# Performance work log

Measured on AMD Instinct MI355X. Metric: run time of the kernel, lower is better.

## Reference

```python
import jax, jax.numpy as jnp
import numpy as np
import math

IN_FEATURES = 256
OUT_FEATURES = 128
B, N = 4, 4096


def setup_inputs() -> dict:
    key = jax.random.key(0)
    ks = jax.random.split(key, 8)
    h = jax.random.normal(ks[0], (B, N, IN_FEATURES), dtype=jnp.float32)
    adj = jax.random.randint(ks[1], (B, N, N), 0, 2, dtype=jnp.int32)
    # Linear params (torch nn.Linear: y = x @ W.T + b)
    s = 1.0 / math.sqrt(IN_FEATURES)
    Wq = jax.random.uniform(ks[2], (OUT_FEATURES, IN_FEATURES), jnp.float32, -s, s)
    bq = jax.random.uniform(ks[3], (OUT_FEATURES,), jnp.float32, -s, s)
    Wk = jax.random.uniform(ks[4], (OUT_FEATURES, IN_FEATURES), jnp.float32, -s, s)
    bk = jax.random.uniform(ks[5], (OUT_FEATURES,), jnp.float32, -s, s)
    Wv = jax.random.uniform(ks[6], (OUT_FEATURES, IN_FEATURES), jnp.float32, -s, s)
    bv = jax.random.uniform(ks[7], (OUT_FEATURES,), jnp.float32, -s, s)
    return {"h": h, "adj": adj, "Wq": Wq, "bq": bq, "Wk": Wk, "bk": bk, "Wv": Wv, "bv": bv}


def reference(h, adj, Wq, bq, Wk, bk, Wv, bv):
    # QKV projections: [B, N, D]
    q = jnp.einsum('bnf,df->bnd', h, Wq) + bq
    k = jnp.einsum('bnf,df->bnd', h, Wk) + bk
    v = jnp.einsum('bnf,df->bnd', h, Wv) + bv
    # Dense scores [B, N, N], scaled
    scores = jnp.einsum('bnd,bmd->bnm', q, k) / math.sqrt(OUT_FEATURES)
    neg = jnp.float32(-9e15)
    scores = jnp.where(adj > 0, scores, neg)
    probs = jax.nn.softmax(scores, axis=-1)
    return jnp.einsum('bnm,bmd->bnd', probs, v)
```

## Files before the change

kernel.cpp:

```cpp
#include <hip/hip_runtime.h>
#include <stdint.h>
#include <math.h>

#define NB 4
#define NN 4096
#define NF 256
#define ND 128
#define KVB 32
#define NR (NB * NN)
#define QKVE ((size_t)NR * ND)

typedef __bf16 bf16x8 __attribute__((ext_vector_type(8)));
typedef __bf16 bf16x4v __attribute__((ext_vector_type(4)));
typedef float f32x4 __attribute__((ext_vector_type(4)));
typedef int i32x4 __attribute__((ext_vector_type(4)));
typedef unsigned short u16x4 __attribute__((ext_vector_type(4)));

__device__ __forceinline__ unsigned short f2bf(float f) {
    union { float f; uint32_t u; } v; v.f = f;
    uint32_t r = (v.u + 0x7FFFu + ((v.u >> 16) & 1u)) >> 16;
    return (unsigned short)r;
}
__device__ __forceinline__ bf16x8 lds_read16(const unsigned short* base, int byte_off) {
    return *reinterpret_cast<const bf16x8*>(reinterpret_cast<const char*>(base) + byte_off);
}
__device__ __forceinline__ void gld_lds16(const void* g, void* l) {
    __builtin_amdgcn_global_load_lds(
        (const __attribute__((address_space(1))) void*)g,
        (__attribute__((address_space(3))) void*)l, 16, 0, 0);
}

__global__ __launch_bounds__(256) void qkv_proj(
    const float* __restrict__ h,
    const float* __restrict__ Wq, const float* __restrict__ bq,
    const float* __restrict__ Wk, const float* __restrict__ bk,
    const float* __restrict__ Wv, const float* __restrict__ bv,
    unsigned short* __restrict__ qo, unsigned short* __restrict__ ko,
    unsigned short* __restrict__ vs, float qscale)
{
    __shared__ unsigned short h_lds[64 * 128];
    __shared__ unsigned short w_lds[128 * 128];

    const int tid = threadIdx.x;
    const int lane = tid & 63;
    const int proj = blockIdx.x >> 8;
    const int R0 = (blockIdx.x & 255) * 64;
    const int wv = tid >> 6;
    const int l15 = lane & 15;
    const int lhi = lane >> 4;

    const float* W    = proj == 0 ? Wq : (proj == 1 ? Wk : Wv);
    const float* bias = proj == 0 ? bq : (proj == 1 ? bk : bv);
    const float scale = proj == 0 ? qscale : 1.0f;

    f32x4 acc[8];
#pragma unroll
    for (int i = 0; i < 8; ++i) acc[i] = f32x4{0.f, 0.f, 0.f, 0.f};

    for (int kc = 0; kc < 2; ++kc) {
        const int c0 = kc * 128;
        __syncthreads();
#pragma unroll
        for (int p = 0; p < 8; ++p) {
            int i2 = p * 256 + tid;
            int row = i2 >> 5;
            int seg = i2 & 31;
            f32x4 hv = *reinterpret_cast<const f32x4*>(h + (size_t)(R0 + row) * NF + c0 + seg * 4);
            u16x4 hb;
            hb[0] = f2bf(hv[0]); hb[1] = f2bf(hv[1]); hb[2] = f2bf(hv[2]); hb[3] = f2bf(hv[3]);
            int byte = (row * 256 + seg * 8) ^ ((row & 7) << 4);
            *reinterpret_cast<u16x4*>(reinterpret_cast<char*>(h_lds) + byte) = hb;
        }
#pragma unroll
        for (int p = 0; p < 16; ++p) {
            int i2 = p * 256 + tid;
            int row = i2 >> 5;
            int seg = i2 & 31;
            f32x4 wv4 = *reinterpret_cast<const f32x4*>(W + (size_t)row * NF + c0 + seg * 4);
            u16x4 wb;
            wb[0] = f2bf(wv4[0]); wb[1] = f2bf(wv4[1]); wb[2] = f2bf(wv4[2]); wb[3] = f2bf(wv4[3]);
            int byte = (row * 256 + seg * 8) ^ ((row & 7) << 4);
            *reinterpret_cast<u16x4*>(reinterpret_cast<char*>(w_lds) + byte) = wb;
        }
        __syncthreads();
        const int arow = 16 * wv + l15;
#pragma unroll
        for (int ks = 0; ks < 4; ++ks) {
            int k = ks * 32 + 8 * lhi;
            bf16x8 a = lds_read16(h_lds, (arow * 256 + k * 2) ^ ((arow & 7) << 4));
#pragma unroll
            for (int cs = 0; cs < 8; ++cs) {
                int d = 16 * cs + l15;
                bf16x8 b = lds_read16(w_lds, (d * 256 + k * 2) ^ ((d & 7) << 4));
                acc[cs] = __builtin_amdgcn_mfma_f32_16x16x32_bf16(a, b, acc[cs], 0, 0, 0);
            }
        }
    }
    if (proj < 2) {
        unsigned short* out = proj == 0 ? qo : ko;
#pragma unroll
        for (int cs = 0; cs < 8; ++cs) {
            int d = 16 * cs + l15;
            float bb = bias[d];
#pragma unroll
            for (int j = 0; j < 4; ++j) {
                int row = R0 + 16 * wv + 4 * lhi + j;
                out[(size_t)row * ND + d] = f2bf((acc[cs][j] + bb) * scale);
            }
        }
    } else {
        const int bb_ = R0 >> 12;
        const int nb_ = (R0 & (NN - 1)) + 16 * wv + 4 * lhi;
        const int pt = nb_ >> 5;
        const int ch = (nb_ >> 3) & 3;
        const int mm0 = nb_ & 7;
#pragma unroll
        for (int cs = 0; cs < 8; ++cs) {
            int d = 16 * cs + l15;
            float bb = bias[d];
            u16x4 o;
#pragma unroll
            for (int j = 0; j < 4; ++j) o[j] = f2bf(acc[cs][j] + bb);
            size_t oidx = ((size_t)(bb_ * 128 + pt)) * 4096 + ch * 1024 + d * 8 + mm0;
            *reinterpret_cast<u16x4*>(vs + oidx) = o;
        }
    }
}

__global__ __launch_bounds__(256, 2) void attn(
    const unsigned short* __restrict__ Q,
    const unsigned short* __restrict__ K,
    const unsigned short* __restrict__ VS,
    const int* __restrict__ adj,
    float* __restrict__ out,
    float* __restrict__ opart1,
    float* __restrict__ ml,
    int ntl)
{
    __shared__ unsigned short stA[8192];
    __shared__ unsigned short stB[8192];
    __shared__ unsigned short p_lds[4096];

    const int tid = threadIdx.x;
    const int lane = tid & 63;
    const int w = tid >> 6;
    const int l15 = lane & 15;
    const int lhi = lane >> 4;

    const int flat = blockIdx.x;
    const int x = flat & 7;
    const int rest = flat >> 3;
    const int qt = rest & 31;
    const int s2 = rest >> 5;
    const int combo = x + 8 * s2;
    const int b = combo & 3;
    const int sp = combo >> 2;
    const int q0w = qt * 128 + w * 32;
    const size_t bN = (size_t)b * NN;
    const int ptbase = sp * ntl;

    const unsigned short* Kb = K + bN * ND;
    const unsigned short* Vbase = VS + (size_t)b * 128 * 4096;
    const int* adjb = adj + (size_t)b * NN * NN + (size_t)(q0w + l15) * NN + 4 * lhi;

    bf16x8 qf[2][4];
#pragma unroll
    for (int g = 0; g < 2; ++g)
#pragma unroll
        for (int ks = 0; ks < 4; ++ks)
            qf[g][ks] = *reinterpret_cast<const bf16x8*>(
                Q + (bN + q0w + g * 16 + l15) * ND + ks * 32 + 8 * lhi);

    f32x4 acc[2][8];
#pragma unroll
    for (int g = 0; g < 2; ++g)
#pragma unroll
        for (int i = 0; i < 8; ++i) acc[g][i] = f32x4{0.f, 0.f, 0.f, 0.f};
    float m_run[2] = {-INFINITY, -INFINITY};
    float l_part[2] = {0.f, 0.f};

    auto stage = [&](unsigned short* st, int pt) {
        const int m0 = pt * KVB;
#pragma unroll
        for (int i = 0; i < 4; ++i) {
            int c = w * 4 + i;
            if (c < 8) {
                int ms = c >> 2, ks = c & 3;
                const unsigned short* src = Kb
                    + (size_t)(m0 + ms * 16 + l15) * ND + ks * 32 + lhi * 8;
                gld_lds16(src, st + c * 512);
            } else {
                int vi = c - 8;
                const unsigned short* src = Vbase + (size_t)pt * 4096 + vi * 512 + lane * 8;
                gld_lds16(src, st + 4096 + vi * 512);
            }
        }
    };
    auto adjld = [&](i32x4 (&ma)[2][2], int pt) {
        const int m0 = pt * KVB;
#pragma unroll
        for (int g = 0; g < 2; ++g)
#pragma unroll
            for (int ms = 0; ms < 2; ++ms)
                ma[g][ms] = *reinterpret_cast<const i32x4*>(
                    adjb + (size_t)(g * 16) * NN + m0 + 16 * ms);
    };

    auto compute = [&](const unsigned short* st, const i32x4 (&ma)[2][2]) {
        bf16x8 kf[2][4];
#pragma unroll
        for (int ms = 0; ms < 2; ++ms)
#pragma unroll
            for (int ks = 0; ks < 4; ++ks)
                kf[ms][ks] = lds_read16(st, (ms * 4 + ks) * 1024 + lane * 16);

        f32x4 s[2][2];
#pragma unroll
        for (int g = 0; g < 2; ++g)
#pragma unroll
            for (int ms = 0; ms < 2; ++ms) s[g][ms] = f32x4{0.f, 0.f, 0.f, 0.f};
        __builtin_amdgcn_s_setprio(1);
#pragma unroll
        for (int g = 0; g < 2; ++g)
#pragma unroll
            for (int ms = 0; ms < 2; ++ms)
#pragma unroll
                for (int ks = 0; ks < 4; ++ks)
                    s[g][ms] = __builtin_amdgcn_mfma_f32_16x16x32_bf16(
                        kf[ms][ks], qf[g][ks], s[g][ms], 0, 0, 0);
        __builtin_amdgcn_s_setprio(0);

        bf16x8 vf[8];
#pragma unroll
        for (int ds = 0; ds < 8; ++ds)
            vf[ds] = lds_read16(st + 4096, lhi * 2048 + ds * 256 + l15 * 16);

        float smaxl[2];
        float dmax = -INFINITY;
#pragma unroll
        for (int g = 0; g < 2; ++g) {
#pragma unroll
            for (int ms = 0; ms < 2; ++ms)
#pragma unroll
                for (int r = 0; r < 4; ++r)
                    if (ma[g][ms][r] == 0) s[g][ms][r] = -1.0e30f;
            float mx = fmaxf(fmaxf(fmaxf(s[g][0][0], s[g][0][1]), fmaxf(s[g][0][2], s[g][0][3])),
                             fmaxf(fmaxf(s[g][1][0], s[g][1][1]), fmaxf(s[g][1][2], s[g][1][3])));
            smaxl[g] = mx;
            dmax = fmaxf(dmax, mx - m_run[g]);
        }
        if (!__all(dmax <= 8.0f)) {
#pragma unroll
            for (int g = 0; g < 2; ++g) {
                float mx = smaxl[g];
                mx = fmaxf(mx, __shfl_xor(mx, 16, 64));
                mx = fmaxf(mx, __shfl_xor(mx, 32, 64));
                float mnew = fmaxf(m_run[g], mx);
                float c = exp2f(m_run[g] - mnew);
                m_run[g] = mnew;
                l_part[g] *= c;
#pragma unroll
                for (int ds = 0; ds < 8; ++ds) acc[g][ds] *= c;
            }
        }

#pragma unroll
        for (int g = 0; g < 2; ++g) {
            bf16x4v pbv[2];
#pragma unroll
            for (int ms = 0; ms < 2; ++ms)
#pragma unroll
                for (int r = 0; r < 4; ++r) {
                    float p = exp2f(s[g][ms][r] - m_run[g]);
                    __bf16 pb = (__bf16)p;
                    l_part[g] += (float)pb;
                    pbv[ms][r] = pb;
                }
            const int base = (w * 2 + g) * 1024 + l15 * 64;
#pragma unroll
            for (int ms = 0; ms < 2; ++ms)
                *reinterpret_cast<bf16x4v*>(reinterpret_cast<char*>(p_lds)
                    + base + ms * 32 + lhi * 8) = pbv[ms];
            bf16x8 pa = lds_read16(p_lds, base + lhi * 16);
            __builtin_amdgcn_s_setprio(1);
#pragma unroll
            for (int ds = 0; ds < 8; ++ds)
                acc[g][ds] = __builtin_amdgcn_mfma_f32_16x16x32_bf16(
                    vf[ds], pa, acc[g][ds], 0, 0, 0);
            __builtin_amdgcn_s_setprio(0);
        }
    };

    i32x4 maskA[2][2], maskB[2][2];
    stage(stA, ptbase);
    adjld(maskA, ptbase);
    __syncthreads();

    for (int t = 0; t < ntl; t += 2) {
        stage(stB, ptbase + t + 1);
        adjld(maskB, ptbase + t + 1);
        compute(stA, maskA);
        __syncthreads();
        int t2 = (t + 2 < ntl) ? t + 2 : ntl - 1;
        stage(stA, ptbase + t2);
        adjld(maskA, ptbase + t2);
        compute(stB, maskB);
        __syncthreads();
    }

#pragma unroll
    for (int g = 0; g < 2; ++g) {
        float rs = l_part[g];
        rs += __shfl_xor(rs, 16, 64);
        rs += __shfl_xor(rs, 32, 64);
        l_part[g] = rs;
    }

    float* op = (sp == 0) ? out : (opart1 + (size_t)(sp - 1) * NR * ND);
#pragma unroll
    for (int g = 0; g < 2; ++g) {
        const size_t rowbase = (bN + q0w + g * 16 + l15) * ND;
#pragma unroll
        for (int ds = 0; ds < 8; ++ds)
            *reinterpret_cast<f32x4*>(op + rowbase + 16 * ds + 4 * lhi) = acc[g][ds];
    }
    if (lhi == 0) {
#pragma unroll
        for (int g = 0; g < 2; ++g) {
            size_t gr = bN + q0w + g * 16 + l15;
            *reinterpret_cast<float2*>(ml + ((size_t)sp * NR + gr) * 2) =
                make_float2(m_run[g], l_part[g]);
        }
    }
}

__global__ __launch_bounds__(256) void merge_splits(
    float* __restrict__ out, const float* __restrict__ opart1,
    const float* __restrict__ ml, int nsplit)
{
    int idx = blockIdx.x * 256 + threadIdx.x;
    int row = idx >> 5;
    int d4 = (idx & 31) * 4;
    float mmax = ml[(size_t)row * 2];
    for (int sp = 1; sp < nsplit; ++sp)
        mmax = fmaxf(mmax, ml[((size_t)sp * NR + row) * 2]);
    f32x4 o0 = *reinterpret_cast<const f32x4*>(out + (size_t)row * ND + d4);
    float w0 = exp2f(ml[(size_t)row * 2] - mmax);
    float lsum = ml[(size_t)row * 2 + 1] * w0;
    f32x4 acc;
#pragma unroll
    for (int j = 0; j < 4; ++j) acc[j] = o0[j] * w0;
    for (int sp = 1; sp < nsplit; ++sp) {
        float m_s = ml[((size_t)sp * NR + row) * 2];
        float l_s = ml[((size_t)sp * NR + row) * 2 + 1];
        float ws_ = exp2f(m_s - mmax);
        f32x4 os = *reinterpret_cast<const f32x4*>(opart1 + ((size_t)(sp - 1) * NR + row) * ND + d4);
#pragma unroll
        for (int j = 0; j < 4; ++j) acc[j] += os[j] * ws_;
        lsum += l_s * ws_;
    }
    float inv = 1.0f / lsum;
    f32x4 r;
#pragma unroll
    for (int j = 0; j < 4; ++j) r[j] = acc[j] * inv;
    *reinterpret_cast<f32x4*>(out + (size_t)row * ND + d4) = r;
}

extern "C" void kernel_launch(void* const* d_in, const int* in_sizes, int n_in,
                              void* d_out, int out_size, void* d_ws, size_t ws_size,
                              hipStream_t stream) {
    const float* h  = (const float*)d_in[0];
    const int* adj  = (const int*)d_in[1];
    const float* Wq = (const float*)d_in[2];
    const float* bq = (const float*)d_in[3];
    const float* Wk = (const float*)d_in[4];
    const float* bk = (const float*)d_in[5];
    const float* Wv = (const float*)d_in[6];
    const float* bv = (const float*)d_in[7];
    float* out = (float*)d_out;

    unsigned short* qws  = (unsigned short*)d_ws;
    unsigned short* kws  = qws + QKVE;
    unsigned short* vsws = kws + QKVE;
    float* opart1 = (float*)(vsws + QKVE);

    const size_t need4 = 3 * QKVE * 2 + 3 * QKVE * 4 + 4 * (size_t)NR * 2 * 4;
    const int nsplit = (ws_size >= need4) ? 4 : 2;
    float* mlws = opart1 + (size_t)(nsplit - 1) * NR * ND;
    const int ntl = (NN / KVB) / nsplit;

    const float qscale = (float)(0.08838834764831845 / 0.6931471805599453);

    qkv_proj<<<dim3(768), 256, 0, stream>>>(
        h, Wq, bq, Wk, bk, Wv, bv, qws, kws, vsws, qscale);
    attn<<<dim3(32 * 4 * nsplit), 256, 0, stream>>>(
        qws, kws, vsws, adj, out, opart1, mlws, ntl);
    merge_splits<<<dim3(NR * 32 / 256), 256, 0, stream>>>(out, opart1, mlws, nsplit);
}
```

Before: 124.6 us.

## Double the attention KV tile and pack the adjacency mask into bitmasks

Raises the attention key/value tile from 32 to 64 rows, doubling the LDS staging buffers and P scratch. QK^T is now computed per key sub-block, and each V fragment read from LDS feeds both query groups, so fewer LDS reads and barriers are spent per key processed. Adjacency loads use nontemporal hints and are packed into per-group bitmasks one tile ahead, which cuts the registers held across tiles. The cost is higher LDS use per block (about 80KB), which may limit occupancy, and more live score registers.

Result: slower. 145.3 us (+16.7%).

```diff
diff --git a/kernel.cpp b/kernel.cpp
--- a/kernel.cpp
+++ b/kernel.cpp
@@ -6,7 +6,7 @@
 #define NN 4096
 #define NF 256
 #define ND 128
-#define KVB 32
+#define KVB 64
 #define NR (NB * NN)
 #define QKVE ((size_t)NR * ND)
 
@@ -28,6 +28,9 @@
     __builtin_amdgcn_global_load_lds(
         (const __attribute__((address_space(1))) void*)g,
         (__attribute__((address_space(3))) void*)l, 16, 0, 0);
+}
+__device__ __forceinline__ i32x4 nt_load4(const int* p) {
+    return __builtin_nontemporal_load(reinterpret_cast<const i32x4*>(p));
 }
 
 __global__ __launch_bounds__(256) void qkv_proj(
@@ -137,9 +140,9 @@
     float* __restrict__ ml,
     int ntl)
 {
-    __shared__ unsigned short stA[8192];
-    __shared__ unsigned short stB[8192];
-    __shared__ unsigned short p_lds[4096];
+    __shared__ unsigned short stA[16384];
+    __shared__ unsigned short stB[16384];
+    __shared__ unsigned short p_lds[8192];
 
     const int tid = threadIdx.x;
     const int lane = tid & 63;
@@ -182,70 +185,78 @@
     auto stage = [&](unsigned short* st, int pt) {
         const int m0 = pt * KVB;
 #pragma unroll
-        for (int i = 0; i < 4; ++i) {
-            int c = w * 4 + i;
-            if (c < 8) {
+        for (int i = 0; i < 8; ++i) {
+            int c = w * 8 + i;
+            if (c < 16) {
                 int ms = c >> 2, ks = c & 3;
                 const unsigned short* src = Kb
                     + (size_t)(m0 + ms * 16 + l15) * ND + ks * 32 + lhi * 8;
                 gld_lds16(src, st + c * 512);
             } else {
-                int vi = c - 8;
-                const unsigned short* src = Vbase + (size_t)pt * 4096 + vi * 512 + lane * 8;
-                gld_lds16(src, st + 4096 + vi * 512);
+                int vi = c - 16;
+                const unsigned short* src = Vbase + (size_t)pt * 8192 + vi * 512 + lane * 8;
+                gld_lds16(src, st + 8192 + vi * 512);
             }
         }
     };
-    auto adjld = [&](i32x4 (&ma)[2][2], int pt) {
+    auto adjld = [&](i32x4 (&raw)[2][4], int pt) {
         const int m0 = pt * KVB;
 #pragma unroll
         for (int g = 0; g < 2; ++g)
 #pragma unroll
-            for (int ms = 0; ms < 2; ++ms)
-                ma[g][ms] = *reinterpret_cast<const i32x4*>(
-                    adjb + (size_t)(g * 16) * NN + m0 + 16 * ms);
+            for (int ms = 0; ms < 4; ++ms)
+                raw[g][ms] = nt_load4(adjb + (size_t)(g * 16) * NN + m0 + 16 * ms);
     };
 
-    auto compute = [&](const unsigned short* st, const i32x4 (&ma)[2][2]) {
-        bf16x8 kf[2][4];
-#pragma unroll
-        for (int ms = 0; ms < 2; ++ms)
+    i32x4 rawm[2][4];
+
+    auto compute = [&](const unsigned short* st, int ptn) {
+        unsigned int mk[2];
+#pragma unroll
+        for (int g = 0; g < 2; ++g) {
+            unsigned int bits = 0;
+#pragma unroll
+            for (int ms = 0; ms < 4; ++ms)
+#pragma unroll
+                for (int r = 0; r < 4; ++r)
+                    bits |= (rawm[g][ms][r] != 0 ? 1u : 0u) << (4 * ms + r);
+            mk[g] = bits;
+        }
+        adjld(rawm, ptn);
+
+        f32x4 s[2][4];
+#pragma unroll
+        for (int g = 0; g < 2; ++g)
+#pragma unroll
+            for (int ms = 0; ms < 4; ++ms) s[g][ms] = f32x4{0.f, 0.f, 0.f, 0.f};
+        __builtin_amdgcn_s_setprio(1);
+#pragma unroll
+        for (int ms = 0; ms < 4; ++ms) {
+            bf16x8 kf[4];
 #pragma unroll
             for (int ks = 0; ks < 4; ++ks)
-                kf[ms][ks] = lds_read16(st, (ms * 4 + ks) * 1024 + lane * 16);
-
-        f32x4 s[2][2];
-#pragma unroll
-        for (int g = 0; g < 2; ++g)
-#pragma unroll
-            for (int ms = 0; ms < 2; ++ms) s[g][ms] = f32x4{0.f, 0.f, 0.f, 0.f};
-        __builtin_amdgcn_s_setprio(1);
-#pragma unroll
-        for (int g = 0; g < 2; ++g)
-#pragma unroll
-            for (int ms = 0; ms < 2; ++ms)
+                kf[ks] = lds_read16(st, (ms * 4 + ks) * 1024 + lane * 16);
+#pragma unroll
+            for (int g = 0; g < 2; ++g)
 #pragma unroll
                 for (int ks = 0; ks < 4; ++ks)
                     s[g][ms] = __builtin_amdgcn_mfma_f32_16x16x32_bf16(
-                        kf[ms][ks], qf[g][ks], s[g][ms], 0, 0, 0);
+                        kf[ks], qf[g][ks], s[g][ms], 0, 0, 0);
+        }
         __builtin_amdgcn_s_setprio(0);
-
-        bf16x8 vf[8];
-#pragma unroll
-        for (int ds = 0; ds < 8; ++ds)
-            vf[ds] = lds_read16(st + 4096, lhi * 2048 + ds * 256 + l15 * 16);
 
         float smaxl[2];
         float dmax = -INFINITY;
 #pragma unroll
         for (int g = 0; g < 2; ++g) {
-#pragma unroll
-            for (int ms = 0; ms < 2; ++ms)
-#pragma unroll
-                for (int r = 0; r < 4; ++r)
-                    if (ma[g][ms][r] == 0) s[g][ms][r] = -1.0e30f;
-            float mx = fmaxf(fmaxf(fmaxf(s[g][0][0], s[g][0][1]), fmaxf(s[g][0][2], s[g][0][3])),
-                             fmaxf(fmaxf(s[g][1][0], s[g][1][1]), fmaxf(s[g][1][2], s[g][1][3])));
+            float mx = -INFINITY;
+#pragma unroll
+            for (int ms = 0; ms < 4; ++ms)
+#pragma unroll
+                for (int r = 0; r < 4; ++r) {
+                    if (!((mk[g] >> (4 * ms + r)) & 1u)) s[g][ms][r] = -1.0e30f;
+                    mx = fmaxf(mx, s[g][ms][r]);
+                }
             smaxl[g] = mx;
             dmax = fmaxf(dmax, mx - m_run[g]);
         }
@@ -264,11 +275,12 @@
             }
         }
 
+        bf16x8 pa[2][2];
 #pragma unroll
         for (int g = 0; g < 2; ++g) {
-            bf16x4v pbv[2];
-#pragma unroll
-            for (int ms = 0; ms < 2; ++ms)
+            bf16x4v pbv[4];
+#pragma unroll
+            for (int ms = 0; ms < 4; ++ms)
 #pragma unroll
                 for (int r = 0; r < 4; ++r) {
                     float p = exp2f(s[g][ms][r] - m_run[g]);
@@ -276,35 +288,41 @@
                     l_part[g] += (float)pb;
                     pbv[ms][r] = pb;
                 }
-            const int base = (w * 2 + g) * 1024 + l15 * 64;
-#pragma unroll
-            for (int ms = 0; ms < 2; ++ms)
+            const int base = (w * 2 + g) * 2048 + l15 * 128;
+#pragma unroll
+            for (int ms = 0; ms < 4; ++ms)
                 *reinterpret_cast<bf16x4v*>(reinterpret_cast<char*>(p_lds)
                     + base + ms * 32 + lhi * 8) = pbv[ms];
-            bf16x8 pa = lds_read16(p_lds, base + lhi * 16);
-            __builtin_amdgcn_s_setprio(1);
-#pragma unroll
-            for (int ds = 0; ds < 8; ++ds)
-                acc[g][ds] = __builtin_amdgcn_mfma_f32_16x16x32_bf16(
-                    vf[ds], pa, acc[g][ds], 0, 0, 0);
-            __builtin_amdgcn_s_setprio(0);
-        }
+            pa[g][0] = lds_read16(p_lds, base + lhi * 16);
+            pa[g][1] = lds_read16(p_lds, base + 64 + lhi * 16);
+        }
+
+        __builtin_amdgcn_s_setprio(1);
+#pragma unroll
+        for (int kwin = 0; kwin < 2; ++kwin)
+#pragma unroll
+            for (int ds = 0; ds < 8; ++ds) {
+                bf16x8 vf = lds_read16(st + 8192 + kwin * 4096,
+                                       lhi * 2048 + ds * 256 + l15 * 16);
+#pragma unroll
+                for (int g = 0; g < 2; ++g)
+                    acc[g][ds] = __builtin_amdgcn_mfma_f32_16x16x32_bf16(
+                        vf, pa[g][kwin], acc[g][ds], 0, 0, 0);
+            }
+        __builtin_amdgcn_s_setprio(0);
     };
 
-    i32x4 maskA[2][2], maskB[2][2];
     stage(stA, ptbase);
-    adjld(maskA, ptbase);
+    adjld(rawm, ptbase);
     __syncthreads();
 
     for (int t = 0; t < ntl; t += 2) {
         stage(stB, ptbase + t + 1);
-        adjld(maskB, ptbase + t + 1);
-        compute(stA, maskA);
+        compute(stA, ptbase + t + 1);
         __syncthreads();
         int t2 = (t + 2 < ntl) ? t + 2 : ntl - 1;
         stage(stA, ptbase + t2);
-        adjld(maskA, ptbase + t2);
-        compute(stB, maskB);
+        compute(stB, ptbase + t2);
         __syncthreads();
     }
 
```
